# Kernel tuning notes

Measured on AMD Instinct MI355X. Metric: run time of the kernel, lower is better.

The kernel has to match this reference:

```python
import jax, jax.numpy as jnp
import numpy as np


def setup_inputs() -> dict:
    key = jax.random.key(0)
    k1, k2 = jax.random.split(key)
    B, C_in, C_out, H, W = 16, 64, 64, 256, 256
    MH, MW = 8, 12
    x = jax.random.normal(k1, (B, C_in, H, W), dtype=jnp.float32)
    scale = 1.0 / np.sqrt(C_in * C_out).astype(np.float32)
    weight = scale * jax.random.normal(k2, (C_in, C_out, MH, MW, 2), dtype=jnp.float32)
    return {"x": x, "weight": weight}


def reference(x, weight):
    B, C, H, W = x.shape
    Wr = W // 2 + 1  # rfft width
    mh = min(weight.shape[2], H)
    mw = min(weight.shape[3], Wr)
    # FFT to frequency domain (orthonormal), keep only low-frequency block
    x_ft = jnp.fft.rfft2(x, norm='ortho')  # (B, C_in, H, Wr) complex
    w_cplx = (weight[..., 0] + 1j * weight[..., 1])[:, :, :mh, :mw]  # (C_in, C_out, mh, mw)
    out_modes = jnp.einsum('bixy,ioxy->boxy', x_ft[:, :, :mh, :mw], w_cplx)
    out_ft = jnp.zeros((B, weight.shape[1], H, Wr), dtype=out_modes.dtype)
    out_ft = out_ft.at[:, :, :mh, :mw].set(out_modes)
    return jnp.fft.irfft2(out_ft, s=(H, W), norm='ortho')
```

## Files before the change

### kernel.cpp

```cpp
#include <hip/hip_runtime.h>
#include <math.h>

#define PI2 6.2831853071795864769f


__global__ __launch_bounds__(256) void k1_fwd(const float* __restrict__ x,
                                              float* __restrict__ Xm) {
  __shared__ float lds[2][4096];
  const int img  = blockIdx.x;
  const int wv   = threadIdx.x >> 6;
  const int lane = threadIdx.x & 63;
  const int h0   = wv * 64;

  float cr[8], sr[8], Cs[8], Ss[8];
#pragma unroll
  for (int ky = 0; ky < 8; ++ky) {
    float th0 = PI2 * (float)((ky * h0) & 255) * (1.0f / 256.0f);
    __sincosf(th0, &sr[ky], &cr[ky]);
    float dth = PI2 * (float)ky * (1.0f / 256.0f);
    __sincosf(dth, &Ss[ky], &Cs[ky]);
  }

  float aR[8][4], aI[8][4];
#pragma unroll
  for (int ky = 0; ky < 8; ++ky)
#pragma unroll
    for (int j = 0; j < 4; ++j) { aR[ky][j] = 0.0f; aI[ky][j] = 0.0f; }

  const float* xp = x + (size_t)img * 65536 + (size_t)h0 * 256 + lane * 4;
#pragma unroll 4
  for (int it = 0; it < 64; ++it) {
    float4 xv = *(const float4*)xp;
    xp += 256;
#pragma unroll
    for (int ky = 0; ky < 8; ++ky) {
      float c = cr[ky], s = sr[ky];
      aR[ky][0] = fmaf(xv.x,  c, aR[ky][0]);  aI[ky][0] = fmaf(xv.x, -s, aI[ky][0]);
      aR[ky][1] = fmaf(xv.y,  c, aR[ky][1]);  aI[ky][1] = fmaf(xv.y, -s, aI[ky][1]);
      aR[ky][2] = fmaf(xv.z,  c, aR[ky][2]);  aI[ky][2] = fmaf(xv.z, -s, aI[ky][2]);
      aR[ky][3] = fmaf(xv.w,  c, aR[ky][3]);  aI[ky][3] = fmaf(xv.w, -s, aI[ky][3]);
      cr[ky] = fmaf(c, Cs[ky], -s * Ss[ky]);
      sr[ky] = fmaf(s, Cs[ky],  c * Ss[ky]);
    }
  }

  if (wv < 2) {
#pragma unroll
    for (int ky = 0; ky < 8; ++ky)
#pragma unroll
      for (int j = 0; j < 4; ++j) {
        int p = (ky * 256 + lane * 4 + j) * 2;
        lds[wv][p] = aR[ky][j];
        lds[wv][p + 1] = aI[ky][j];
      }
  }
  __syncthreads();
  if (wv >= 2) {
#pragma unroll
    for (int ky = 0; ky < 8; ++ky)
#pragma unroll
      for (int j = 0; j < 4; ++j) {
        int p = (ky * 256 + lane * 4 + j) * 2;
        lds[wv - 2][p] += aR[ky][j];
        lds[wv - 2][p + 1] += aI[ky][j];
      }
  }
  __syncthreads();
  for (int f = threadIdx.x; f < 4096; f += 256) lds[0][f] += lds[1][f];
  __syncthreads();

  if (threadIdx.x < 96) {
    int ky = threadIdx.x / 12, kx = threadIdx.x % 12;
    float Cw, Sw;
    __sincosf(PI2 * (float)kx * (1.0f / 256.0f), &Sw, &Cw);
    float c = 1.0f, s = 0.0f, Xr = 0.0f, Xi = 0.0f;
    const float* base = &lds[0][ky * 512];
    for (int w = 0; w < 256; ++w) {
      float Sre = base[w * 2], Sim = base[w * 2 + 1];
      Xr += Sre * c + Sim * s;
      Xi += Sim * c - Sre * s;
      float nc = fmaf(c, Cw, -s * Sw);
      s = fmaf(s, Cw, c * Sw);
      c = nc;
    }
    Xm[((size_t)img * 96 + threadIdx.x) * 2]     = Xr * (1.0f / 256.0f);
    Xm[((size_t)img * 96 + threadIdx.x) * 2 + 1] = Xi * (1.0f / 256.0f);
  }
}

__global__ __launch_bounds__(256) void k3_mix(const float* __restrict__ Xm,
                                              const float* __restrict__ wt,
                                              float* __restrict__ Fm) {
  __shared__ float Xs[1024 * 2];
  __shared__ float Ws[4096 * 2];
  const int pos = blockIdx.x;
  for (int idx = threadIdx.x; idx < 1024; idx += 256) {
    Xs[idx * 2]     = Xm[((size_t)idx * 96 + pos) * 2];
    Xs[idx * 2 + 1] = Xm[((size_t)idx * 96 + pos) * 2 + 1];
  }
  for (int idx = threadIdx.x; idx < 4096; idx += 256) {
    Ws[idx * 2]     = wt[((size_t)idx * 96 + pos) * 2];
    Ws[idx * 2 + 1] = wt[((size_t)idx * 96 + pos) * 2 + 1];
  }
  __syncthreads();
  const int b = threadIdx.x >> 4;
  const int og = (threadIdx.x & 15) * 4;
  float ar[4] = {0, 0, 0, 0}, ai[4] = {0, 0, 0, 0};
  for (int i = 0; i < 64; ++i) {
    float xr = Xs[(b * 64 + i) * 2], xi = Xs[(b * 64 + i) * 2 + 1];
#pragma unroll
    for (int r = 0; r < 4; ++r) {
      float wr = Ws[(i * 64 + og + r) * 2], wi = Ws[(i * 64 + og + r) * 2 + 1];
      ar[r] += xr * wr - xi * wi;
      ai[r] += xr * wi + xi * wr;
    }
  }
#pragma unroll
  for (int r = 0; r < 4; ++r) {
    Fm[((size_t)(b * 64 + og + r) * 96 + pos) * 2]     = ar[r];
    Fm[((size_t)(b * 64 + og + r) * 96 + pos) * 2 + 1] = ai[r];
  }
}

__global__ __launch_bounds__(256) void k4a_invh(const float* __restrict__ Fm,
                                                float* __restrict__ U) {
  __shared__ float Fs[192];
  const int img2 = blockIdx.x;
  if (threadIdx.x < 192) Fs[threadIdx.x] = Fm[(size_t)img2 * 192 + threadIdx.x];
  __syncthreads();
  const int h = threadIdx.x;
  float cc[8], ss[8];
#pragma unroll
  for (int ky = 0; ky < 8; ++ky) {
    float th = PI2 * (float)((ky * h) & 255) * (1.0f / 256.0f);
    __sincosf(th, &ss[ky], &cc[ky]);
  }
  float4 ov4[6];
  float* ov = (float*)ov4;
#pragma unroll
  for (int kx = 0; kx < 12; ++kx) {
    float Ur = 0.0f, Ui = 0.0f;
#pragma unroll
    for (int ky = 0; ky < 8; ++ky) {
      float Fr = Fs[(ky * 12 + kx) * 2], Fi = Fs[(ky * 12 + kx) * 2 + 1];
      Ur += Fr * cc[ky] - Fi * ss[ky];
      Ui += Fr * ss[ky] + Fi * cc[ky];
    }
    float a = (kx == 0 ? 1.0f : 2.0f) * (1.0f / 256.0f);
    ov[kx * 2] = Ur * a;
    ov[kx * 2 + 1] = Ui * a;
  }
  float4* dst = (float4*)(U + ((size_t)img2 * 256 + h) * 24);
#pragma unroll
  for (int k = 0; k < 6; ++k) dst[k] = ov4[k];
}

__global__ __launch_bounds__(256) void k4b_invw(const float* __restrict__ U,
                                                float* __restrict__ outp) {
  const int wid = blockIdx.x * 4 + (threadIdx.x >> 6);
  const int lane = threadIdx.x & 63;
  float c[12][4], s[12][4];
#pragma unroll
  for (int kx = 0; kx < 12; ++kx)
#pragma unroll
    for (int j = 0; j < 4; ++j) {
      float th = PI2 * (float)((kx * (lane * 4 + j)) & 255) * (1.0f / 256.0f);
      __sincosf(th, &s[kx][j], &c[kx][j]);
    }
  for (int r = 0; r < 64; ++r) {
    const int row = wid * 64 + r;
    float4 u4[6];
    const float4* us = (const float4*)(U + (size_t)row * 24);
#pragma unroll
    for (int k = 0; k < 6; ++k) u4[k] = us[k];
    const float* u = (const float*)u4;
    float acc0 = 0, acc1 = 0, acc2 = 0, acc3 = 0;
#pragma unroll
    for (int kx = 0; kx < 12; ++kx) {
      float ur = u[kx * 2], ui = u[kx * 2 + 1];
      acc0 = fmaf(ur, c[kx][0], fmaf(-ui, s[kx][0], acc0));
      acc1 = fmaf(ur, c[kx][1], fmaf(-ui, s[kx][1], acc1));
      acc2 = fmaf(ur, c[kx][2], fmaf(-ui, s[kx][2], acc2));
      acc3 = fmaf(ur, c[kx][3], fmaf(-ui, s[kx][3], acc3));
    }
    float4 o = {acc0, acc1, acc2, acc3};
    *(float4*)(outp + (size_t)row * 256 + lane * 4) = o;
  }
}

extern "C" void kernel_launch(void* const* d_in, const int* in_sizes, int n_in,
                              void* d_out, int out_size, void* d_ws, size_t ws_size,
                              hipStream_t stream) {
  const float* x  = (const float*)d_in[0];
  const float* wt = (const float*)d_in[1];
  float* outp = (float*)d_out;

  float* Xm = (float*)d_ws;
  float* Fm = Xm + 196608;
  float* U  = Fm + 196608;

  k1_fwd  <<<1024, 256, 0, stream>>>(x, Xm);
  k3_mix  <<<  96, 256, 0, stream>>>(Xm, wt, Fm);
  k4a_invh<<<1024, 256, 0, stream>>>(Fm, U);
  k4b_invw<<<1024, 256, 0, stream>>>(U, outp);
}
```

Before: 585.8 us.

## Fold row pairs via even/odd symmetry, tabulate twiddles, transpose mode layout

The forward kernel pairs row h with row h+128 and uses the symmetry that even ky sees their sum and odd ky their difference. This halves the row-DFT multiply-adds, and twiddles now come from a shared-memory table instead of a recurrence. The mode buffer is written position-major so the mixing kernel can read it contiguously. The inverse-width kernel is remapped to one thread per column with scalar stores across all 256 rows, trading float4 stores for less twiddle register pressure.

```diff
diff --git a/kernel.cpp b/kernel.cpp
--- a/kernel.cpp
+++ b/kernel.cpp
@@ -6,20 +6,26 @@
 
 __global__ __launch_bounds__(256) void k1_fwd(const float* __restrict__ x,
                                               float* __restrict__ Xm) {
+  __shared__ float tw[128][16];
   __shared__ float lds[2][4096];
   const int img  = blockIdx.x;
   const int wv   = threadIdx.x >> 6;
   const int lane = threadIdx.x & 63;
-  const int h0   = wv * 64;
-
-  float cr[8], sr[8], Cs[8], Ss[8];
-#pragma unroll
-  for (int ky = 0; ky < 8; ++ky) {
-    float th0 = PI2 * (float)((ky * h0) & 255) * (1.0f / 256.0f);
-    __sincosf(th0, &sr[ky], &cr[ky]);
-    float dth = PI2 * (float)ky * (1.0f / 256.0f);
-    __sincosf(dth, &Ss[ky], &Cs[ky]);
-  }
+
+  {
+    int h = threadIdx.x >> 1;
+    int kyb = (threadIdx.x & 1) * 4;
+#pragma unroll
+    for (int j = 0; j < 4; ++j) {
+      int ky = kyb + j;
+      float th = PI2 * (float)((ky * h) & 255) * (1.0f / 256.0f);
+      float s_, c_;
+      __sincosf(th, &s_, &c_);
+      tw[h][ky * 2] = c_;
+      tw[h][ky * 2 + 1] = -s_;
+    }
+  }
+  __syncthreads();
 
   float aR[8][4], aI[8][4];
 #pragma unroll
@@ -27,20 +33,26 @@
 #pragma unroll
     for (int j = 0; j < 4; ++j) { aR[ky][j] = 0.0f; aI[ky][j] = 0.0f; }
 
-  const float* xp = x + (size_t)img * 65536 + (size_t)h0 * 256 + lane * 4;
-#pragma unroll 4
-  for (int it = 0; it < 64; ++it) {
-    float4 xv = *(const float4*)xp;
-    xp += 256;
+  const float* xa = x + (size_t)img * 65536 + (size_t)(wv * 32) * 256 + lane * 4;
+  const float* xb = xa + 128 * 256;
+  for (int it = 0; it < 32; ++it) {
+    const int h = wv * 32 + it;
+    float4 va = *(const float4*)xa;
+    float4 vb = *(const float4*)xb;
+    xa += 256; xb += 256;
+    float p0 = va.x + vb.x, p1 = va.y + vb.y, p2 = va.z + vb.z, p3 = va.w + vb.w;
+    float m0 = va.x - vb.x, m1 = va.y - vb.y, m2 = va.z - vb.z, m3 = va.w - vb.w;
 #pragma unroll
     for (int ky = 0; ky < 8; ++ky) {
-      float c = cr[ky], s = sr[ky];
-      aR[ky][0] = fmaf(xv.x,  c, aR[ky][0]);  aI[ky][0] = fmaf(xv.x, -s, aI[ky][0]);
-      aR[ky][1] = fmaf(xv.y,  c, aR[ky][1]);  aI[ky][1] = fmaf(xv.y, -s, aI[ky][1]);
-      aR[ky][2] = fmaf(xv.z,  c, aR[ky][2]);  aI[ky][2] = fmaf(xv.z, -s, aI[ky][2]);
-      aR[ky][3] = fmaf(xv.w,  c, aR[ky][3]);  aI[ky][3] = fmaf(xv.w, -s, aI[ky][3]);
-      cr[ky] = fmaf(c, Cs[ky], -s * Ss[ky]);
-      sr[ky] = fmaf(s, Cs[ky],  c * Ss[ky]);
+      float c  = tw[h][ky * 2];
+      float ns = tw[h][ky * 2 + 1];
+      float u0, u1, u2, u3;
+      if (ky & 1) { u0 = m0; u1 = m1; u2 = m2; u3 = m3; }
+      else        { u0 = p0; u1 = p1; u2 = p2; u3 = p3; }
+      aR[ky][0] = fmaf(u0, c, aR[ky][0]);  aI[ky][0] = fmaf(u0, ns, aI[ky][0]);
+      aR[ky][1] = fmaf(u1, c, aR[ky][1]);  aI[ky][1] = fmaf(u1, ns, aI[ky][1]);
+      aR[ky][2] = fmaf(u2, c, aR[ky][2]);  aI[ky][2] = fmaf(u2, ns, aI[ky][2]);
+      aR[ky][3] = fmaf(u3, c, aR[ky][3]);  aI[ky][3] = fmaf(u3, ns, aI[ky][3]);
     }
   }
 
@@ -83,8 +95,8 @@
       s = fmaf(s, Cw, c * Sw);
       c = nc;
     }
-    Xm[((size_t)img * 96 + threadIdx.x) * 2]     = Xr * (1.0f / 256.0f);
-    Xm[((size_t)img * 96 + threadIdx.x) * 2 + 1] = Xi * (1.0f / 256.0f);
+    float2 v = { Xr * (1.0f / 256.0f), Xi * (1.0f / 256.0f) };
+    ((float2*)Xm)[(size_t)threadIdx.x * 1024 + img] = v;
   }
 }
 
@@ -94,10 +106,8 @@
   __shared__ float Xs[1024 * 2];
   __shared__ float Ws[4096 * 2];
   const int pos = blockIdx.x;
-  for (int idx = threadIdx.x; idx < 1024; idx += 256) {
-    Xs[idx * 2]     = Xm[((size_t)idx * 96 + pos) * 2];
-    Xs[idx * 2 + 1] = Xm[((size_t)idx * 96 + pos) * 2 + 1];
-  }
+  for (int idx = threadIdx.x; idx < 2048; idx += 256)
+    Xs[idx] = Xm[(size_t)pos * 2048 + idx];
   for (int idx = threadIdx.x; idx < 4096; idx += 256) {
     Ws[idx * 2]     = wt[((size_t)idx * 96 + pos) * 2];
     Ws[idx * 2 + 1] = wt[((size_t)idx * 96 + pos) * 2 + 1];
@@ -157,34 +167,29 @@
 
 __global__ __launch_bounds__(256) void k4b_invw(const float* __restrict__ U,
                                                 float* __restrict__ outp) {
-  const int wid = blockIdx.x * 4 + (threadIdx.x >> 6);
-  const int lane = threadIdx.x & 63;
-  float c[12][4], s[12][4];
-#pragma unroll
-  for (int kx = 0; kx < 12; ++kx)
-#pragma unroll
-    for (int j = 0; j < 4; ++j) {
-      float th = PI2 * (float)((kx * (lane * 4 + j)) & 255) * (1.0f / 256.0f);
-      __sincosf(th, &s[kx][j], &c[kx][j]);
-    }
-  for (int r = 0; r < 64; ++r) {
-    const int row = wid * 64 + r;
+  const int img2 = blockIdx.x;
+  const int w = threadIdx.x;
+  float c[12], ns[12];
+#pragma unroll
+  for (int kx = 0; kx < 12; ++kx) {
+    float th = PI2 * (float)((kx * w) & 255) * (1.0f / 256.0f);
+    float s_;
+    __sincosf(th, &s_, &c[kx]);
+    ns[kx] = -s_;
+  }
+  const float* ub = U + (size_t)img2 * 6144;
+  float* ob = outp + (size_t)img2 * 65536 + w;
+  for (int h = 0; h < 256; ++h) {
     float4 u4[6];
-    const float4* us = (const float4*)(U + (size_t)row * 24);
+    const float4* us = (const float4*)(ub + h * 24);
 #pragma unroll
     for (int k = 0; k < 6; ++k) u4[k] = us[k];
     const float* u = (const float*)u4;
-    float acc0 = 0, acc1 = 0, acc2 = 0, acc3 = 0;
-#pragma unroll
-    for (int kx = 0; kx < 12; ++kx) {
-      float ur = u[kx * 2], ui = u[kx * 2 + 1];
-      acc0 = fmaf(ur, c[kx][0], fmaf(-ui, s[kx][0], acc0));
-      acc1 = fmaf(ur, c[kx][1], fmaf(-ui, s[kx][1], acc1));
-      acc2 = fmaf(ur, c[kx][2], fmaf(-ui, s[kx][2], acc2));
-      acc3 = fmaf(ur, c[kx][3], fmaf(-ui, s[kx][3], acc3));
-    }
-    float4 o = {acc0, acc1, acc2, acc3};
-    *(float4*)(outp + (size_t)row * 256 + lane * 4) = o;
+    float acc = 0.0f;
+#pragma unroll
+    for (int kx = 0; kx < 12; ++kx)
+      acc = fmaf(u[kx * 2], c[kx], fmaf(u[kx * 2 + 1], ns[kx], acc));
+    ob[h * 256] = acc;
   }
 }
 
```

Result: faster. 542.7 us (-7.4%).
